# Optimization experiments

Measured on AMD Instinct MI355X. Metric: run time of the kernel, lower is better.

Reference implementation:

```python
import jax, jax.numpy as jnp
import numpy as np

EPS = 1e-8


def normalize_points(p):
    # p: [..., D+1]; normalize feature part to unit L2 norm, fix sign by last coord
    f = p[..., :-1]
    h = p[..., -1:]
    zero_mask = jnp.all(f == 0, axis=-1, keepdims=True)
    f = jnp.where(zero_mask, jnp.ones_like(f), f)
    norm = jnp.linalg.norm(f, axis=-1, keepdims=True)
    nf = f / jnp.clip(norm, EPS)
    n = jnp.concatenate([nf, h], axis=-1)
    sign = jnp.sign(n[..., -1:])
    sign = jnp.where(sign == 0, jnp.ones_like(sign), sign)
    return n * sign


def uhg_transform(x, weight):
    # x: [M, D_in+1], weight: [D_out, D_in]
    f = x[..., :-1]
    h = x[..., -1:]
    t = jnp.matmul(f, weight.T)  # [M, D_out]
    norm = jnp.linalg.norm(t, axis=-1, keepdims=True)
    t = t / jnp.clip(norm, EPS)
    return normalize_points(jnp.concatenate([t, h], axis=-1))


def setup_inputs() -> dict:
    key = jax.random.key(0)
    k1, k2, k3, k4 = jax.random.split(key, 4)
    N, E = 20000, 320000
    D_IN, D_OUT = 256, 256  # in_features-1, out_features
    x = jax.random.normal(k1, (N, D_IN + 1), dtype=jnp.float32)
    edge_index = jax.random.randint(k2, (2, E), 0, N, dtype=jnp.int32)
    # orthogonal-ish init approximated by row-normalized gaussian weights
    W_self = jax.random.normal(k3, (D_OUT, D_IN), dtype=jnp.float32)
    W_self = W_self / jnp.clip(jnp.linalg.norm(W_self, axis=1, keepdims=True), EPS)
    W_neigh = jax.random.normal(k4, (D_OUT, D_IN), dtype=jnp.float32)
    W_neigh = W_neigh / jnp.clip(jnp.linalg.norm(W_neigh, axis=1, keepdims=True), EPS)
    return {"x": x, "W_self": W_self, "W_neigh": W_neigh, "edge_index": edge_index}


def reference(x, W_self, W_neigh, edge_index):
    N = x.shape[0]
    D_OUT = W_self.shape[0]
    x = normalize_points(x)
    row, col = edge_index[0], edge_index[1]

    self_trans = uhg_transform(x, W_self)              # [N, D_OUT+1]
    neigh_trans = uhg_transform(x[col], W_neigh)       # [E, D_OUT+1]

    # mean aggregation: scatter-add full (features + homogeneous), count-divide features only
    out = jnp.zeros((N, D_OUT + 1), dtype=x.dtype).at[:, -1].set(1.0)
    out = out.at[row].add(neigh_trans)
    count = jnp.zeros((N, 1), dtype=x.dtype).at[row].add(1.0)
    count = jnp.clip(count, 1.0)
    out = jnp.concatenate([out[:, :-1] / count, out[:, -1:]], axis=-1)
    out = normalize_points(out)

    # uhg_weighted_average(p1, p2, 0.5): elementwise blend then renormalize
    t = jnp.clip(0.5 / (1.0 - 0.5 + EPS), EPS, 1e8)
    p1 = normalize_points(self_trans)
    p2 = normalize_points(out)
    avg = (p1 * t + p2) / jnp.clip(t + 1.0, EPS)
    combined = normalize_points(avg)
    return normalize_points(combined)
```

## Files before the change

### kernel.cpp

```cpp
#include <hip/hip_runtime.h>
#include <hip/hip_bf16.h>

#define EPSF 1e-8f
#define CAP 64

typedef __attribute__((ext_vector_type(4))) float floatx4;
typedef __attribute__((ext_vector_type(2))) float floatx2;
typedef __attribute__((ext_vector_type(2))) long longx2;

__device__ inline unsigned short f2bf(float v) {
    union { float f; unsigned int u; } un; un.f = v;
    unsigned int r = (un.u + 0x7fffu + ((un.u >> 16) & 1u)) >> 16;
    return (unsigned short)r;
}
__device__ inline float bf2f(unsigned short u) {
    union { unsigned int i; float f; } un; un.i = ((unsigned int)u) << 16;
    return un.f;
}

__device__ inline unsigned char f2fp8(float v) {
#if __has_builtin(__builtin_amdgcn_cvt_pk_fp8_f32)
    return (unsigned char)(__builtin_amdgcn_cvt_pk_fp8_f32(v, 0.f, 0u, false) & 0xff);
#else
    union { float f; unsigned u; } x; x.f = v;
    unsigned s = x.u >> 31; x.u &= 0x7fffffffu;
    if (x.f != x.f || x.f == 0.f) return (unsigned char)(s << 7);
    int e = (int)((x.u >> 23) & 0xff) - 127 + 7;
    unsigned m = x.u & 0x7fffffu;
    unsigned char r;
    if (e >= 1) {
        unsigned keep = m >> 20, rest = m & 0xfffffu;
        keep += (rest > 0x80000u) || (rest == 0x80000u && (keep & 1));
        if (keep == 8) { keep = 0; e += 1; }
        if (e > 15) { e = 15; keep = 6; }
        r = (unsigned char)((e << 3) | keep);
    } else {
        int q = (int)(x.f * 512.f + 0.5f);
        if (q > 7) r = 0x08; else r = (unsigned char)q;
    }
    return (unsigned char)(r | (s << 7));
#endif
}
__device__ inline unsigned pk_fp8x4(float v0, float v1, float v2, float v3) {
#if __has_builtin(__builtin_amdgcn_cvt_pk_fp8_f32)
    unsigned u = __builtin_amdgcn_cvt_pk_fp8_f32(v0, v1, 0u, false);
    u = __builtin_amdgcn_cvt_pk_fp8_f32(v2, v3, u, true);
    return u;
#else
    return (unsigned)f2fp8(v0) | ((unsigned)f2fp8(v1) << 8)
         | ((unsigned)f2fp8(v2) << 16) | ((unsigned)f2fp8(v3) << 24);
#endif
}
__device__ inline floatx2 fp8x2_to_f32(unsigned int u, bool word) {
#if __has_builtin(__builtin_amdgcn_cvt_pk_f32_fp8)
    return word ? __builtin_amdgcn_cvt_pk_f32_fp8(u, true)
                : __builtin_amdgcn_cvt_pk_f32_fp8(u, false);
#else
    floatx2 out;
    #pragma unroll
    for (int i = 0; i < 2; ++i) {
        unsigned char b = (u >> ((word ? 16 : 0) + 8 * i)) & 0xff;
        unsigned s = (b >> 7) & 1, e = (b >> 3) & 15, m = b & 7;
        float v;
        if (e) { union { unsigned u2; float f; } x; x.u2 = (s << 31) | ((e + 120u) << 23) | (m << 20); v = x.f; }
        else   { v = (s ? -1.f : 1.f) * (float)m * 0.001953125f; }
        out[i] = v;
    }
    return out;
#endif
}

__device__ inline void acc16(float* acc, uint4 u) {
    floatx2 p;
    p = fp8x2_to_f32(u.x, false); acc[0]  += p[0]; acc[1]  += p[1];
    p = fp8x2_to_f32(u.x, true);  acc[2]  += p[0]; acc[3]  += p[1];
    p = fp8x2_to_f32(u.y, false); acc[4]  += p[0]; acc[5]  += p[1];
    p = fp8x2_to_f32(u.y, true);  acc[6]  += p[0]; acc[7]  += p[1];
    p = fp8x2_to_f32(u.z, false); acc[8]  += p[0]; acc[9]  += p[1];
    p = fp8x2_to_f32(u.z, true);  acc[10] += p[0]; acc[11] += p[1];
    p = fp8x2_to_f32(u.w, false); acc[12] += p[0]; acc[13] += p[1];
    p = fp8x2_to_f32(u.w, true);  acc[14] += p[0]; acc[15] += p[1];
}

__global__ __launch_bounds__(512) void k_front(
        const float* __restrict__ x, const float* __restrict__ Ws,
        const float* __restrict__ Wn,
        unsigned char* __restrict__ Wswz,
        float* __restrict__ xh, int* __restrict__ cnt, int N) {
    int b = blockIdx.x, t = threadIdx.x;
    if (b < 32) {
        int idx = b * 512 + t;
        int t0 = (idx & 3) * 4;
        int lane = (idx >> 2) & 63;
        int p = (idx >> 8) & 3;
        int g = (idx >> 10) & 3;
        int wq = (idx >> 12) & 3;
        int q = lane >> 4, l16 = lane & 15;
        int row = wq * 64 + g * 16 + l16;
        int s = 2 * p + (t0 >> 3);
        int k0 = 32 * s + 8 * q + (t0 & 7);
        float4 vs = *reinterpret_cast<const float4*>(Ws + row * 256 + k0);
        float4 vn = *reinterpret_cast<const float4*>(Wn + row * 256 + k0);
        reinterpret_cast<unsigned*>(Wswz)[idx] = pk_fp8x4(vs.x, vs.y, vs.z, vs.w);
        reinterpret_cast<unsigned*>(Wswz)[16384 + idx] = pk_fp8x4(vn.x, vn.y, vn.z, vn.w);
    } else {
        int i = (b - 32) * 512 + t;
        if (i < N) {
            xh[i] = fabsf(x[(size_t)i * 257 + 256]);
            cnt[i] = 0;
        }
    }
}

__global__ __launch_bounds__(512, 4) void k_mid(
        const float* __restrict__ x,
        const unsigned char* __restrict__ Wswz,
        const int* __restrict__ ei,
        int* __restrict__ cnt, unsigned short* __restrict__ scol,
        unsigned short* __restrict__ selfb, unsigned char* __restrict__ yb8,
        int N, int E, int EB) {
    int b = blockIdx.x, tid = threadIdx.x;
    int T = gridDim.x;

    int ebBefore = (int)(((long)b * EB) / T);
    bool isBucket = ((int)(((long)(b + 1) * EB) / T)) != ebBefore;
    if (isBucket) {
        int e0 = ebBefore * 2048 + tid;
        int rr[4], cc[4];
        bool ok[4];
        #pragma unroll
        for (int j = 0; j < 4; ++j) {
            int e = e0 + j * 512;
            ok[j] = (e < E);
            rr[j] = ok[j] ? ei[e] : 0;
            cc[j] = ok[j] ? ei[E + e] : 0;
        }
        #pragma unroll
        for (int j = 0; j < 4; ++j) {
            if (ok[j]) {
                int pos = atomicAdd(&cnt[rr[j]], 1);
                if (pos < CAP) scol[rr[j] * CAP + pos] = (unsigned short)cc[j];
            }
        }
        return;
    }

    int wave = tid >> 6, lane = tid & 63;
    int quad = lane >> 4, l16 = lane & 15;
    int mat = wave >> 2, rg = wave & 3;
    int row0 = (b - ebBefore) * 64;
    int rbase = row0 + rg * 16;

    int ga = rbase + l16; if (ga >= N) ga = N - 1;
    const float* xr = x + (size_t)ga * 257;
    float h = xr[256];
    float sg = (h < 0.f) ? -1.f : 1.f;

    long af[8];
    #pragma unroll
    for (int s = 0; s < 8; ++s) {
        const float* px = xr + 32 * s + 8 * quad;
        float4 u0 = *reinterpret_cast<const float4*>(px);
        float4 u1 = *reinterpret_cast<const float4*>(px + 4);
        unsigned lo = pk_fp8x4(u0.x * sg, u0.y * sg, u0.z * sg, u0.w * sg);
        unsigned hi = pk_fp8x4(u1.x * sg, u1.y * sg, u1.z * sg, u1.w * sg);
        union { unsigned u2[2]; long l; } cv; cv.u2[0] = lo; cv.u2[1] = hi;
        af[s] = cv.l;
    }

    const unsigned char* Wm = Wswz + ((size_t)mat << 16);
    floatx4 acc[16];
    #pragma unroll
    for (int G = 0; G < 16; ++G) acc[G] = floatx4{0.f, 0.f, 0.f, 0.f};

    #pragma unroll
    for (int G = 0; G < 16; ++G) {
        const unsigned char* Wb = Wm + ((size_t)(G >> 2) << 14);
        int g = G & 3;
        #pragma unroll
        for (int p = 0; p < 4; ++p) {
            longx2 w = *reinterpret_cast<const longx2*>(
                Wb + (((g * 4 + p) * 64 + lane) << 4));
            acc[G] = __builtin_amdgcn_mfma_f32_16x16x32_fp8_fp8(af[2 * p],     w[0], acc[G], 0, 0, 0);
            acc[G] = __builtin_amdgcn_mfma_f32_16x16x32_fp8_fp8(af[2 * p + 1], w[1], acc[G], 0, 0, 0);
        }
    }

    #pragma unroll
    for (int reg = 0; reg < 4; ++reg) {
        int gr = rbase + quad * 4 + reg;
        float ps = 0.f;
        #pragma unroll
        for (int G = 0; G < 16; ++G) ps += acc[G][reg] * acc[G][reg];
        ps += __shfl_xor(ps, 1, 64);
        ps += __shfl_xor(ps, 2, 64);
        ps += __shfl_xor(ps, 4, 64);
        ps += __shfl_xor(ps, 8, 64);
        bool zero = (ps == 0.f);
        float scale = zero ? 0.f : (1.f / fmaxf(sqrtf(ps), EPSF));
        if (gr < N) {
            #pragma unroll
            for (int G = 0; G < 16; ++G) {
                int col = (G >> 2) * 64 + (G & 3) * 16 + l16;
                float val = zero ? 0.0625f : acc[G][reg] * scale;
                if (mat == 0) selfb[(size_t)gr * 256 + col] = f2bf(val);
                else          yb8[(size_t)gr * 256 + col]  = f2fp8(val);
            }
        }
    }
}

__global__ __launch_bounds__(256) void k_agg_combine(
        const int* __restrict__ cnt, const unsigned short* __restrict__ scol,
        const unsigned char* __restrict__ yb8,
        const float* __restrict__ xh,
        const unsigned short* __restrict__ selfb,
        float* __restrict__ out, int N) {
    int wid = (blockIdx.x * 256 + threadIdx.x) >> 6;
    if (wid >= N) return;
    int lane = threadIdx.x & 63;
    int g = lane >> 4, l16 = lane & 15;
    int deg = cnt[wid]; if (deg > CAP) deg = CAP;
    int beg = wid * CAP;

    int cv = (lane < deg) ? (int)scol[beg + lane] : 0;
    float hv = (lane < deg) ? xh[cv] : 0.f;

    const unsigned short* sp = selfb + (size_t)wid * 256 + l16 * 16;
    uint4 s0 = *reinterpret_cast<const uint4*>(sp);
    uint4 s1 = *reinterpret_cast<const uint4*>(sp + 8);

    float acc[16];
    #pragma unroll
    for (int j = 0; j < 16; ++j) acc[j] = 0.f;

    int e = 0;
    for (; e + 16 <= deg; e += 16) {
        int c0 = __shfl(cv, e + g, 64);
        int c1 = __shfl(cv, e + 4 + g, 64);
        int c2 = __shfl(cv, e + 8 + g, 64);
        int c3 = __shfl(cv, e + 12 + g, 64);
        uint4 u0 = *reinterpret_cast<const uint4*>(yb8 + (size_t)c0 * 256 + l16 * 16);
        uint4 u1 = *reinterpret_cast<const uint4*>(yb8 + (size_t)c1 * 256 + l16 * 16);
        uint4 u2 = *reinterpret_cast<const uint4*>(yb8 + (size_t)c2 * 256 + l16 * 16);
        uint4 u3 = *reinterpret_cast<const uint4*>(yb8 + (size_t)c3 * 256 + l16 * 16);
        acc16(acc, u0); acc16(acc, u1); acc16(acc, u2); acc16(acc, u3);
    }
    for (; e + 4 <= deg; e += 4) {
        int c0 = __shfl(cv, e + g, 64);
        uint4 u0 = *reinterpret_cast<const uint4*>(yb8 + (size_t)c0 * 256 + l16 * 16);
        acc16(acc, u0);
    }
    {
        int rem = deg - e;
        int ct = __shfl(cv, e + g, 64);
        if (g < rem) {
            uint4 u0 = *reinterpret_cast<const uint4*>(yb8 + (size_t)ct * 256 + l16 * 16);
            acc16(acc, u0);
        }
    }
    #pragma unroll
    for (int j = 0; j < 16; ++j) {
        acc[j] += __shfl_xor(acc[j], 16, 64);
        acc[j] += __shfl_xor(acc[j], 32, 64);
    }
    float hs = hv;
    #pragma unroll
    for (int o = 32; o > 0; o >>= 1) hs += __shfl_xor(hs, o, 64);

    float cn = (deg > 0) ? (float)deg : 1.f;
    float rcn = 1.f / cn;
    float m_[16];
    float ss = 0.f;
    #pragma unroll
    for (int j = 0; j < 16; ++j) { m_[j] = acc[j] * rcn; ss += m_[j] * m_[j]; }
    #pragma unroll
    for (int o = 1; o < 16; o <<= 1) ss += __shfl_xor(ss, o, 64);
    bool z = (ss == 0.f);
    float inv = 1.f / fmaxf(z ? 16.f : sqrtf(ss), EPSF);

    unsigned sw[8] = { s0.x, s0.y, s0.z, s0.w, s1.x, s1.y, s1.z, s1.w };
    float v_[16];
    float ss2 = 0.f;
    #pragma unroll
    for (int j = 0; j < 8; ++j) {
        float slo = bf2f((unsigned short)(sw[j] & 0xffff));
        float shi = bf2f((unsigned short)(sw[j] >> 16));
        float olo = (z ? 1.f : m_[2 * j]) * inv;
        float ohi = (z ? 1.f : m_[2 * j + 1]) * inv;
        v_[2 * j]     = 0.5f * (slo + olo);
        v_[2 * j + 1] = 0.5f * (shi + ohi);
        ss2 += v_[2 * j] * v_[2 * j] + v_[2 * j + 1] * v_[2 * j + 1];
    }
    #pragma unroll
    for (int o = 1; o < 16; o <<= 1) ss2 += __shfl_xor(ss2, o, 64);
    bool z2 = (ss2 == 0.f);
    float inv2 = 1.f / fmaxf(z2 ? 16.f : sqrtf(ss2), EPSF);

    {
        float* op = out + (size_t)wid * 257 + l16 * 16 + g * 4;
        op[0] = (z2 ? 1.f : v_[g * 4 + 0]) * inv2;
        op[1] = (z2 ? 1.f : v_[g * 4 + 1]) * inv2;
        op[2] = (z2 ? 1.f : v_[g * 4 + 2]) * inv2;
        op[3] = (z2 ? 1.f : v_[g * 4 + 3]) * inv2;
    }
    if (lane == 0) out[(size_t)wid * 257 + 256] = 0.5f * (xh[wid] + 1.f + hs);
}

extern "C" void kernel_launch(void* const* d_in, const int* in_sizes, int n_in,
                              void* d_out, int out_size, void* d_ws, size_t ws_size,
                              hipStream_t stream) {
    const float* x  = (const float*)d_in[0];
    const float* Ws = (const float*)d_in[1];
    const float* Wn = (const float*)d_in[2];
    const int*   ei = (const int*)d_in[3];
    int N = in_sizes[0] / 257;
    int E = in_sizes[3] / 2;
    float* out = (float*)d_out;

    char* ws = (char*)d_ws;
    size_t off = 0;
    auto alloc = [&](size_t bytes) {
        void* p = ws + off;
        off = (off + bytes + 255) & ~(size_t)255;
        return p;
    };
    unsigned char* Wswz = (unsigned char*)alloc(131072);
    float* xh    = (float*)alloc((size_t)N * 4);
    unsigned char* yb8 = (unsigned char*)alloc((size_t)N * 256);
    unsigned short* selfb = (unsigned short*)alloc((size_t)N * 256 * 2);
    int* cnt  = (int*)alloc((size_t)N * 4);
    unsigned short* scol = (unsigned short*)alloc((size_t)N * CAP * 2);

    int XB = (N + 511) / 512;
    hipLaunchKernelGGL(k_front, dim3(32 + XB), dim3(512), 0, stream,
                       x, Ws, Wn, Wswz, xh, cnt, N);
    int GB = (N + 63) / 64, EB = (E + 2047) / 2048;
    hipLaunchKernelGGL(k_mid, dim3(GB + EB), dim3(512), 0, stream,
                       x, Wswz, ei, cnt, scol, selfb, yb8, N, E, EB);
    hipLaunchKernelGGL(k_agg_combine, dim3((N + 3) / 4), dim3(256), 0, stream,
                       cnt, scol, yb8, xh, selfb, out, N);
}
```

Before: 131.6 us.

## Split GEMM columns across waves with shared-memory row-norm reduction

Each k_mid block now handles 16 rows instead of 64, and its four waves per matrix each compute a 64-column quarter rather than all 256 columns for 16 rows. Partial row sums of squares are combined through a small shared array and a block barrier before normalization. Accumulators drop from 16 to 4 floatx4 per lane, so launch bounds rise to 8 blocks per CU. The aim is more occupancy and a larger grid, at the cost of each x row being loaded and converted to fp8 by four waves instead of one, plus an added __syncthreads.

After: 134.4 us. +2.1%, slower.

```diff
diff --git a/kernel.cpp b/kernel.cpp
--- a/kernel.cpp
+++ b/kernel.cpp
@@ -112,13 +112,14 @@
     }
 }
 
-__global__ __launch_bounds__(512, 4) void k_mid(
+__global__ __launch_bounds__(512, 8) void k_mid(
         const float* __restrict__ x,
         const unsigned char* __restrict__ Wswz,
         const int* __restrict__ ei,
         int* __restrict__ cnt, unsigned short* __restrict__ scol,
         unsigned short* __restrict__ selfb, unsigned char* __restrict__ yb8,
         int N, int E, int EB) {
+    __shared__ float pss[8][16];
     int b = blockIdx.x, tid = threadIdx.x;
     int T = gridDim.x;
 
@@ -147,11 +148,10 @@
 
     int wave = tid >> 6, lane = tid & 63;
     int quad = lane >> 4, l16 = lane & 15;
-    int mat = wave >> 2, rg = wave & 3;
-    int row0 = (b - ebBefore) * 64;
-    int rbase = row0 + rg * 16;
-
-    int ga = rbase + l16; if (ga >= N) ga = N - 1;
+    int mat = wave >> 2, colq = wave & 3;
+    int row0 = (b - ebBefore) * 16;
+
+    int ga = row0 + l16; if (ga >= N) ga = N - 1;
     const float* xr = x + (size_t)ga * 257;
     float h = xr[256];
     float sg = (h < 0.f) ? -1.f : 1.f;
@@ -168,41 +168,48 @@
         af[s] = cv.l;
     }
 
-    const unsigned char* Wm = Wswz + ((size_t)mat << 16);
-    floatx4 acc[16];
-    #pragma unroll
-    for (int G = 0; G < 16; ++G) acc[G] = floatx4{0.f, 0.f, 0.f, 0.f};
-
-    #pragma unroll
-    for (int G = 0; G < 16; ++G) {
-        const unsigned char* Wb = Wm + ((size_t)(G >> 2) << 14);
-        int g = G & 3;
+    const unsigned char* Wb = Wswz + ((size_t)mat << 16) + ((size_t)colq << 14);
+    floatx4 acc[4];
+    #pragma unroll
+    for (int g = 0; g < 4; ++g) acc[g] = floatx4{0.f, 0.f, 0.f, 0.f};
+
+    #pragma unroll
+    for (int g = 0; g < 4; ++g) {
         #pragma unroll
         for (int p = 0; p < 4; ++p) {
             longx2 w = *reinterpret_cast<const longx2*>(
                 Wb + (((g * 4 + p) * 64 + lane) << 4));
-            acc[G] = __builtin_amdgcn_mfma_f32_16x16x32_fp8_fp8(af[2 * p],     w[0], acc[G], 0, 0, 0);
-            acc[G] = __builtin_amdgcn_mfma_f32_16x16x32_fp8_fp8(af[2 * p + 1], w[1], acc[G], 0, 0, 0);
+            acc[g] = __builtin_amdgcn_mfma_f32_16x16x32_fp8_fp8(af[2 * p],     w[0], acc[g], 0, 0, 0);
+            acc[g] = __builtin_amdgcn_mfma_f32_16x16x32_fp8_fp8(af[2 * p + 1], w[1], acc[g], 0, 0, 0);
         }
     }
 
     #pragma unroll
     for (int reg = 0; reg < 4; ++reg) {
-        int gr = rbase + quad * 4 + reg;
         float ps = 0.f;
         #pragma unroll
-        for (int G = 0; G < 16; ++G) ps += acc[G][reg] * acc[G][reg];
+        for (int g = 0; g < 4; ++g) ps += acc[g][reg] * acc[g][reg];
         ps += __shfl_xor(ps, 1, 64);
         ps += __shfl_xor(ps, 2, 64);
         ps += __shfl_xor(ps, 4, 64);
         ps += __shfl_xor(ps, 8, 64);
-        bool zero = (ps == 0.f);
-        float scale = zero ? 0.f : (1.f / fmaxf(sqrtf(ps), EPSF));
+        if (l16 == 0) pss[wave][quad * 4 + reg] = ps;
+    }
+    __syncthreads();
+
+    int wb = mat * 4;
+    #pragma unroll
+    for (int reg = 0; reg < 4; ++reg) {
+        int r = quad * 4 + reg;
+        int gr = row0 + r;
+        float ss = pss[wb][r] + pss[wb + 1][r] + pss[wb + 2][r] + pss[wb + 3][r];
+        bool zero = (ss == 0.f);
+        float scale = zero ? 0.f : (1.f / fmaxf(sqrtf(ss), EPSF));
         if (gr < N) {
             #pragma unroll
-            for (int G = 0; G < 16; ++G) {
-                int col = (G >> 2) * 64 + (G & 3) * 16 + l16;
-                float val = zero ? 0.0625f : acc[G][reg] * scale;
+            for (int g = 0; g < 4; ++g) {
+                int col = colq * 64 + g * 16 + l16;
+                float val = zero ? 0.0625f : acc[g][reg] * scale;
                 if (mat == 0) selfb[(size_t)gr * 256 + col] = f2bf(val);
                 else          yb8[(size_t)gr * 256 + col]  = f2fp8(val);
             }
@@ -335,7 +342,7 @@
     int XB = (N + 511) / 512;
     hipLaunchKernelGGL(k_front, dim3(32 + XB), dim3(512), 0, stream,
                        x, Ws, Wn, Wswz, xh, cnt, N);
-    int GB = (N + 63) / 64, EB = (E + 2047) / 2048;
+    int GB = (N + 15) / 16, EB = (E + 2047) / 2048;
     hipLaunchKernelGGL(k_mid, dim3(GB + EB), dim3(512), 0, stream,
                        x, Wswz, ei, cnt, scol, selfb, yb8, N, E, EB);
     hipLaunchKernelGGL(k_agg_combine, dim3((N + 3) / 4), dim3(256), 0, stream,
```

## Move edge bucketing from GEMM kernel into front kernel, memset counts

Applied to the files above, without the earlier changes.

The edge-bucketing work (atomic count plus column scatter) moves out of the interleaved GEMM kernel and into the front kernel as extra blocks. Count zeroing is now done with a hipMemsetAsync before the front kernel. This lets the GEMM kernel run homogeneous blocks without the interleaved bucket blocks and per-block division logic. It adds a memset launch and makes the front kernel heavier, which may lengthen its critical path.

After: 144.8 us. 10.0% more time.

```diff
diff --git a/kernel.cpp b/kernel.cpp
--- a/kernel.cpp
+++ b/kernel.cpp
@@ -84,12 +84,31 @@
 
 __global__ __launch_bounds__(512) void k_front(
         const float* __restrict__ x, const float* __restrict__ Ws,
-        const float* __restrict__ Wn,
-        unsigned char* __restrict__ Wswz,
-        float* __restrict__ xh, int* __restrict__ cnt, int N) {
+        const float* __restrict__ Wn, const int* __restrict__ ei,
+        unsigned char* __restrict__ Wswz, float* __restrict__ xh,
+        int* __restrict__ cnt, unsigned short* __restrict__ scol,
+        int N, int E, int EB) {
     int b = blockIdx.x, t = threadIdx.x;
-    if (b < 32) {
-        int idx = b * 512 + t;
+    if (b < EB) {
+        int e0 = b * 2048 + t;
+        int rr[4], cc[4];
+        bool ok[4];
+        #pragma unroll
+        for (int j = 0; j < 4; ++j) {
+            int e = e0 + j * 512;
+            ok[j] = (e < E);
+            rr[j] = ok[j] ? ei[e] : 0;
+            cc[j] = ok[j] ? ei[E + e] : 0;
+        }
+        #pragma unroll
+        for (int j = 0; j < 4; ++j) {
+            if (ok[j]) {
+                int pos = atomicAdd(&cnt[rr[j]], 1);
+                if (pos < CAP) scol[rr[j] * CAP + pos] = (unsigned short)cc[j];
+            }
+        }
+    } else if (b < EB + 32) {
+        int idx = (b - EB) * 512 + t;
         int t0 = (idx & 3) * 4;
         int lane = (idx >> 2) & 63;
         int p = (idx >> 8) & 3;
@@ -104,51 +123,22 @@
         reinterpret_cast<unsigned*>(Wswz)[idx] = pk_fp8x4(vs.x, vs.y, vs.z, vs.w);
         reinterpret_cast<unsigned*>(Wswz)[16384 + idx] = pk_fp8x4(vn.x, vn.y, vn.z, vn.w);
     } else {
-        int i = (b - 32) * 512 + t;
-        if (i < N) {
-            xh[i] = fabsf(x[(size_t)i * 257 + 256]);
-            cnt[i] = 0;
-        }
+        int i = (b - EB - 32) * 512 + t;
+        if (i < N) xh[i] = fabsf(x[(size_t)i * 257 + 256]);
     }
 }
 
 __global__ __launch_bounds__(512, 4) void k_mid(
         const float* __restrict__ x,
         const unsigned char* __restrict__ Wswz,
-        const int* __restrict__ ei,
-        int* __restrict__ cnt, unsigned short* __restrict__ scol,
         unsigned short* __restrict__ selfb, unsigned char* __restrict__ yb8,
-        int N, int E, int EB) {
+        int N) {
     int b = blockIdx.x, tid = threadIdx.x;
-    int T = gridDim.x;
-
-    int ebBefore = (int)(((long)b * EB) / T);
-    bool isBucket = ((int)(((long)(b + 1) * EB) / T)) != ebBefore;
-    if (isBucket) {
-        int e0 = ebBefore * 2048 + tid;
-        int rr[4], cc[4];
-        bool ok[4];
-        #pragma unroll
-        for (int j = 0; j < 4; ++j) {
-            int e = e0 + j * 512;
-            ok[j] = (e < E);
-            rr[j] = ok[j] ? ei[e] : 0;
-            cc[j] = ok[j] ? ei[E + e] : 0;
-        }
-        #pragma unroll
-        for (int j = 0; j < 4; ++j) {
-            if (ok[j]) {
-                int pos = atomicAdd(&cnt[rr[j]], 1);
-                if (pos < CAP) scol[rr[j] * CAP + pos] = (unsigned short)cc[j];
-            }
-        }
-        return;
-    }
 
     int wave = tid >> 6, lane = tid & 63;
     int quad = lane >> 4, l16 = lane & 15;
     int mat = wave >> 2, rg = wave & 3;
-    int row0 = (b - ebBefore) * 64;
+    int row0 = b * 64;
     int rbase = row0 + rg * 16;
 
     int ga = rbase + l16; if (ga >= N) ga = N - 1;
@@ -332,12 +322,14 @@
     int* cnt  = (int*)alloc((size_t)N * 4);
     unsigned short* scol = (unsigned short*)alloc((size_t)N * CAP * 2);
 
-    int XB = (N + 511) / 512;
-    hipLaunchKernelGGL(k_front, dim3(32 + XB), dim3(512), 0, stream,
-                       x, Ws, Wn, Wswz, xh, cnt, N);
-    int GB = (N + 63) / 64, EB = (E + 2047) / 2048;
-    hipLaunchKernelGGL(k_mid, dim3(GB + EB), dim3(512), 0, stream,
-                       x, Wswz, ei, cnt, scol, selfb, yb8, N, E, EB);
+    hipMemsetAsync(cnt, 0, (size_t)N * 4, stream);
+
+    int XB = (N + 511) / 512, EB = (E + 2047) / 2048;
+    hipLaunchKernelGGL(k_front, dim3(EB + 32 + XB), dim3(512), 0, stream,
+                       x, Ws, Wn, ei, Wswz, xh, cnt, scol, N, E, EB);
+    int GB = (N + 63) / 64;
+    hipLaunchKernelGGL(k_mid, dim3(GB), dim3(512), 0, stream,
+                       x, Wswz, selfb, yb8, N);
     hipLaunchKernelGGL(k_agg_combine, dim3((N + 3) / 4), dim3(256), 0, stream,
                        cnt, scol, yb8, xh, selfb, out, N);
 }
```
